# Kernel optimization log

Measured on AMD Instinct MI355X. Metric: run time of the kernel, lower is better.

Reference implementation:

```python
import jax, jax.numpy as jnp
import numpy as np

M = 16                      # multiplicity of each irrep block
INV3 = 1.0 / np.sqrt(3.0)   # w3j(1,1,0) component-normalized
INV2 = 1.0 / np.sqrt(2.0)   # w3j(1,1,1) component-normalized
A0 = 1.0 / np.sqrt(2.0 * M) # fan-in norm for 0e outputs (2 paths x mul 16)
A1 = 1.0 / np.sqrt(3.0 * M) # fan-in norm for 1o outputs (3 paths x mul 16)


def setup_inputs() -> dict:
    E, N, ED, HID = 100000, 10000, 32, 128
    WNUM = 2 * M * (2 * M) + 3 * M * M  # 1792 per-edge TP weights
    ks = jax.random.split(jax.random.key(0), 10)
    return {
        "dst": jax.random.randint(ks[0], (E,), 0, N),
        "x_src": jax.random.normal(ks[1], (E, 4 * M), jnp.float32),   # 16x0e+16x1o
        "x_dst": jax.random.normal(ks[2], (N, 4 * M), jnp.float32),
        "sh": jax.random.normal(ks[3], (E, 4), jnp.float32),          # 1x0e+1x1o
        "edge_attr": jax.random.normal(ks[4], (E, ED), jnp.float32),
        "We1": jax.random.normal(ks[5], (ED, HID), jnp.float32) / np.sqrt(ED),
        "be1": jnp.zeros((HID,), jnp.float32),
        "We2": jax.random.normal(ks[6], (HID, WNUM), jnp.float32) / np.sqrt(HID),
        "be2": jnp.zeros((WNUM,), jnp.float32),
        "Wr0": jax.random.normal(ks[7], (M, 2 * M), jnp.float32),     # 16x0e -> 32x0e
        "Wr1": jax.random.normal(ks[8], (M, M), jnp.float32),         # 16x1o -> 16x1o
    }


def _forward(dst, x_src, x_dst, sh, edge_attr, We1, be1, We2, be2, Wr0, Wr1):
    E = x_src.shape[0]
    N = x_dst.shape[0]
    o0 = 2 * M  # 32x0e tp output (scalars + gates)

    # edge MLP -> per-edge tensor-product weights [E, 1792]
    w = jax.nn.relu(edge_attr @ We1 + be1) @ We2 + be2
    i = 0
    w_ss = w[:, i:i + M * o0].reshape(E, M, o0); i += M * o0   # 0e x 0e -> 0e
    w_vv0 = w[:, i:i + M * o0].reshape(E, M, o0); i += M * o0  # 1o x 1o -> 0e
    w_sv = w[:, i:i + M * M].reshape(E, M, M); i += M * M      # 0e x 1o -> 1o
    w_vs = w[:, i:i + M * M].reshape(E, M, M); i += M * M      # 1o x 0e -> 1o
    w_vv1 = w[:, i:i + M * M].reshape(E, M, M)                 # 1o x 1o -> 1o

    s1 = x_src[:, :M]                       # [E, 16]
    v1 = x_src[:, M:].reshape(E, M, 3)      # [E, 16, 3]
    s2 = sh[:, 0]                           # [E]
    v2 = sh[:, 1:4]                         # [E, 3]

    # fully-connected tensor product with per-edge weights
    out0 = A0 * (jnp.einsum('em,emo->eo', s1 * s2[:, None], w_ss)
                 + INV3 * jnp.einsum('emc,ec,emo->eo', v1, v2, w_vv0))  # [E, 32]
    cross = jnp.cross(v1, v2[:, None, :])   # [E, 16, 3]
    out1 = A1 * (jnp.einsum('em,ec,emo->eoc', s1, v2, w_sv)
                 + jnp.einsum('emc,e,emo->eoc', v1, s2, w_vs)
                 + INV2 * jnp.einsum('emc,emo->eoc', cross, w_vv1))     # [E, 16, 3]
    msg = jnp.concatenate([out0, out1.reshape(E, -1)], axis=1)          # [E, 80]

    # scatter-mean over destination nodes
    ssum = jax.ops.segment_sum(msg, dst, num_segments=N)
    cnt = jax.ops.segment_sum(jnp.ones((E,), msg.dtype), dst, num_segments=N)
    msg = ssum / jnp.maximum(cnt, 1.0)[:, None]                          # [N, 80]

    # residual equivariant linear on x_dst
    sd = x_dst[:, :M]
    vd = x_dst[:, M:].reshape(N, M, 3)
    res0 = (sd @ Wr0) / np.sqrt(M)                                       # [N, 32]
    res1 = jnp.einsum('nmc,mo->noc', vd, Wr1) / np.sqrt(M)               # [N, 16, 3]
    msg = msg + jnp.concatenate([res0, res1.reshape(N, -1)], axis=1)

    # gate nonlinearity: relu(scalars), sigmoid(gates) * gated vectors
    scalars = jax.nn.relu(msg[:, :M])
    gates = jax.nn.sigmoid(msg[:, M:2 * M])
    gated = msg[:, 2 * M:].reshape(N, M, 3) * gates[:, :, None]
    return jnp.concatenate([scalars, gated.reshape(N, -1)], axis=1)      # [N, 64]


def reference(dst, x_src, x_dst, sh, edge_attr, We1, be1, We2, be2, Wr0, Wr1):
    return _forward(dst, x_src, x_dst, sh, edge_attr, We1, be1, We2, be2, Wr0, Wr1)
```

## Files before the change

### kernel.cpp

```cpp
#include <hip/hip_runtime.h>
#include <math.h>

#define WNUM 1792
#define HID 128

#define INV3C 0.5773502691896258f
#define INV2C 0.7071067811865476f
#define A0C   0.17677669529663687f
#define A1C   0.14433756729740643f
#define MAXDEG 64

typedef short bf8 __attribute__((ext_vector_type(8)));
typedef _Float16 f16x8 __attribute__((ext_vector_type(8)));
typedef _Float16 f16x4 __attribute__((ext_vector_type(4)));
typedef float f32x4 __attribute__((ext_vector_type(4)));

__device__ inline unsigned short f2bf(float f) {
  union { float f; unsigned u; } v; v.f = f;
  unsigned r = v.u + 0x7FFFu + ((v.u >> 16) & 1u);
  return (unsigned short)(r >> 16);
}
__device__ inline float bf2f(unsigned short h) {
  union { unsigned u; float f; } v; v.u = ((unsigned)h) << 16;
  return v.f;
}
__device__ inline float wscale(int t) {
  if (t < 32) return A0C;
  if (t < 64) return A0C * INV3C;
  if (t < 96) return A1C;
  return A1C * INV2C;
}

__global__ __launch_bounds__(256) void prep_kernel(
    const float* __restrict__ We1, const float* __restrict__ We2,
    const float* __restrict__ be2,
    unsigned short* __restrict__ we1x, _Float16* __restrict__ we2h,
    float* __restrict__ be2p, int* __restrict__ cntp, int N)
{
  int i = blockIdx.x * 256 + threadIdx.x;
  if (i < 28672) {
    int t = i >> 8, c = (i >> 6) & 3, lane = i & 63;
    int quad = lane >> 4, l15 = lane & 15;
    int col = t * 16 + l15;
    float sc = wscale(t);
    f16x8 v;
    #pragma unroll
    for (int j = 0; j < 8; ++j) {
      int k = c * 32 + quad * 8 + j;
      v[j] = (_Float16)(We2[(size_t)k * WNUM + col] * sc);
    }
    *(f16x8*)(we2h + (size_t)t * 2048 + c * 512 + lane * 8) = v;
  } else if (i < 29184) {
    int q = i - 28672;
    int c1 = q >> 6, lane = q & 63;
    int quad = lane >> 4, l15 = lane & 15;
    int col = c1 * 16 + l15;
    bf8 hh, ll;
    #pragma unroll
    for (int j = 0; j < 8; ++j) {
      int k = quad * 8 + j;
      float v = We1[k * HID + col];
      unsigned short hi = f2bf(v);
      hh[j] = (short)hi;
      ll[j] = (short)f2bf(v - bf2f(hi));
    }
    *(bf8*)(we1x + c1 * 1024 + lane * 8) = hh;
    *(bf8*)(we1x + c1 * 1024 + 512 + lane * 8) = ll;
  } else if (i < 30976) {
    int q = i - 29184;
    int t = q >> 4, l16 = q & 15;
    be2p[(t >> 1) * 32 + l16 * 2 + (t & 1)] = be2[q] * wscale(t);
  } else if (i < 30976 + N) {
    cntp[i - 30976] = 0;
  }
}

__device__ inline void chains2(const f16x8* a0, const f16x8* a1,
    const f16x8* b, float2 bias, f32x4* wa, f32x4* wb)
{
  f32x4 ca0 = {bias.x, bias.x, bias.x, bias.x};
  f32x4 cb0 = {bias.y, bias.y, bias.y, bias.y};
  f32x4 ca1 = ca0, cb1 = cb0;
  ca0 = __builtin_amdgcn_mfma_f32_16x16x32_f16(a0[0], b[0], ca0, 0, 0, 0);
  cb0 = __builtin_amdgcn_mfma_f32_16x16x32_f16(a0[0], b[4], cb0, 0, 0, 0);
  ca1 = __builtin_amdgcn_mfma_f32_16x16x32_f16(a1[0], b[0], ca1, 0, 0, 0);
  cb1 = __builtin_amdgcn_mfma_f32_16x16x32_f16(a1[0], b[4], cb1, 0, 0, 0);
  ca0 = __builtin_amdgcn_mfma_f32_16x16x32_f16(a0[1], b[1], ca0, 0, 0, 0);
  cb0 = __builtin_amdgcn_mfma_f32_16x16x32_f16(a0[1], b[5], cb0, 0, 0, 0);
  ca1 = __builtin_amdgcn_mfma_f32_16x16x32_f16(a1[1], b[1], ca1, 0, 0, 0);
  cb1 = __builtin_amdgcn_mfma_f32_16x16x32_f16(a1[1], b[5], cb1, 0, 0, 0);
  ca0 = __builtin_amdgcn_mfma_f32_16x16x32_f16(a0[2], b[2], ca0, 0, 0, 0);
  cb0 = __builtin_amdgcn_mfma_f32_16x16x32_f16(a0[2], b[6], cb0, 0, 0, 0);
  ca1 = __builtin_amdgcn_mfma_f32_16x16x32_f16(a1[2], b[2], ca1, 0, 0, 0);
  cb1 = __builtin_amdgcn_mfma_f32_16x16x32_f16(a1[2], b[6], cb1, 0, 0, 0);
  ca0 = __builtin_amdgcn_mfma_f32_16x16x32_f16(a0[3], b[3], ca0, 0, 0, 0);
  cb0 = __builtin_amdgcn_mfma_f32_16x16x32_f16(a0[3], b[7], cb0, 0, 0, 0);
  ca1 = __builtin_amdgcn_mfma_f32_16x16x32_f16(a1[3], b[3], ca1, 0, 0, 0);
  cb1 = __builtin_amdgcn_mfma_f32_16x16x32_f16(a1[3], b[7], cb1, 0, 0, 0);
  wa[0] = ca0; wb[0] = cb0; wa[1] = ca1; wb[1] = cb1;
}

__device__ inline void loadB8(const _Float16* __restrict__ bG, f16x8* b) {
  b[0] = *(const f16x8*)(bG);
  b[1] = *(const f16x8*)(bG + 512);
  b[2] = *(const f16x8*)(bG + 1024);
  b[3] = *(const f16x8*)(bG + 1536);
  b[4] = *(const f16x8*)(bG + 2048);
  b[5] = *(const f16x8*)(bG + 2560);
  b[6] = *(const f16x8*)(bG + 3072);
  b[7] = *(const f16x8*)(bG + 3584);
}

template <bool MSG>
__global__ __launch_bounds__(256, 2) void edge_kernel(
    const float* __restrict__ ea, const float* __restrict__ xsrc,
    const float* __restrict__ sh, const int* __restrict__ dst,
    const float* __restrict__ be1,
    const unsigned short* __restrict__ we1x, const _Float16* __restrict__ we2h,
    const float* __restrict__ be2p,
    float* __restrict__ outp, int* __restrict__ eidx, int* __restrict__ cntp, int E)
{
  const int lane = threadIdx.x & 63;
  const int w    = threadIdx.x >> 6;
  const int quad = lane >> 4;
  const int l16  = lane & 15;
  const int eb   = (blockIdx.x * 4 + w) * 32;

  __shared__ _Float16 h_s[4][16][136];
  __shared__ _Float16 s1h_s[4][16][32];
  __shared__ _Float16 v1h_s[4][16][3][32];
  __shared__ float4 vq_s[4][32];

  if (lane < 32) {
    int ge = eb + lane;
    if (ge < E) {
      int node = dst[ge];
      int pos = atomicAdd(cntp + node, 1);
      if (MSG) { if (pos < MAXDEG) eidx[node * MAXDEG + pos] = ge; }
    }
  }

  {
    int e2 = lane >> 1, mg = lane & 1;
    int ge = eb + e2;
    if (ge < E) {
      const float* xp = xsrc + (size_t)ge * 64;
      float4 sq0 = *(const float4*)(xp + mg * 8);
      float4 sq1 = *(const float4*)(xp + mg * 8 + 4);
      float s1a[8] = {sq0.x,sq0.y,sq0.z,sq0.w,sq1.x,sq1.y,sq1.z,sq1.w};
      const float* vp = xp + 16 + mg * 24;
      float la[24];
      #pragma unroll
      for (int qv = 0; qv < 6; ++qv) {
        float4 t = *(const float4*)(vp + qv * 4);
        la[qv*4+0] = t.x; la[qv*4+1] = t.y; la[qv*4+2] = t.z; la[qv*4+3] = t.w;
      }
      float4 shq = *(const float4*)(sh + (size_t)ge * 4);
      float s2 = shq.x, v2x = shq.y, v2y = shq.z, v2z = shq.w;
      #pragma unroll
      for (int mi = 0; mi < 8; ++mi) {
        int m = mg * 8 + mi;
        float v1x = la[mi*3], v1y = la[mi*3+1], v1z = la[mi*3+2];
        s1h_s[w][m][e2] = (_Float16)s1a[mi];
        v1h_s[w][m][0][e2] = (_Float16)v1x;
        v1h_s[w][m][1][e2] = (_Float16)v1y;
        v1h_s[w][m][2][e2] = (_Float16)v1z;
      }
      if (mg == 0) vq_s[w][e2] = make_float4(v2x, v2y, v2z, s2);
    } else {
      #pragma unroll
      for (int mi = 0; mi < 8; ++mi) {
        int m = mg * 8 + mi;
        s1h_s[w][m][e2] = (_Float16)0.f;
        v1h_s[w][m][0][e2] = (_Float16)0.f;
        v1h_s[w][m][1][e2] = (_Float16)0.f;
        v1h_s[w][m][2][e2] = (_Float16)0.f;
      }
      if (mg == 0) vq_s[w][e2] = make_float4(0,0,0,0);
    }
  }

  f16x8 af[2][4];
  {
    const unsigned short* wb1 = we1x + lane * 8;
    #pragma unroll
    for (int g = 0; g < 2; ++g) {
      bf8 ah, al;
      {
        int gea = eb + g * 16 + l16; if (gea > E - 1) gea = E - 1;
        const float* ep = ea + (size_t)gea * 32 + quad * 8;
        float4 p0 = *(const float4*)ep;
        float4 p1 = *(const float4*)(ep + 4);
        float pv[8] = {p0.x,p0.y,p0.z,p0.w,p1.x,p1.y,p1.z,p1.w};
        #pragma unroll
        for (int j = 0; j < 8; ++j) {
          unsigned short hi = f2bf(pv[j]);
          ah[j] = (short)hi;
          al[j] = (short)f2bf(pv[j] - bf2f(hi));
        }
      }
      #pragma unroll 2
      for (int c = 0; c < 8; ++c) {
        bf8 bh = *(const bf8*)(wb1 + c * 1024);
        bf8 bl = *(const bf8*)(wb1 + c * 1024 + 512);
        float bias = be1[c * 16 + l16];
        f32x4 hc = {bias, bias, bias, bias};
        hc = __builtin_amdgcn_mfma_f32_16x16x32_bf16(al, bh, hc, 0, 0, 0);
        hc = __builtin_amdgcn_mfma_f32_16x16x32_bf16(ah, bl, hc, 0, 0, 0);
        hc = __builtin_amdgcn_mfma_f32_16x16x32_bf16(ah, bh, hc, 0, 0, 0);
        #pragma unroll
        for (int r = 0; r < 4; ++r)
          h_s[w][quad * 4 + r][c * 16 + l16] = (_Float16)fmaxf(hc[r], 0.f);
      }
      #pragma unroll
      for (int ch = 0; ch < 4; ++ch)
        af[g][ch] = *(const f16x8*)&h_s[w][l16][ch * 32 + quad * 8];
      asm volatile("s_waitcnt lgkmcnt(0)" ::: "memory");
      __builtin_amdgcn_sched_barrier(0);
    }
  }

  const float* bp = be2p + l16 * 2;
  const _Float16* bG0 = we2h + lane * 8;
  float m0a[2][4] = {{0,0,0,0},{0,0,0,0}}, m0b[2][4] = {{0,0,0,0},{0,0,0,0}};

  f16x8 bufA[8], bufB[8];
  loadB8(bG0, bufA);

  {
    float s2v[2][4];
    #pragma unroll
    for (int g = 0; g < 2; ++g)
      #pragma unroll
      for (int r = 0; r < 4; ++r)
        s2v[g][r] = vq_s[w][g * 16 + quad * 4 + r].w;

    #pragma unroll 1
    for (int i = 0; i < 16; i += 2) {
      loadB8(bG0 + (size_t)(i + 1) * 4096, bufB);
      f32x4 wa[2], wb[2];
      chains2(af[0], af[1], bufA, *(const float2*)(bp + i * 32), wa, wb);
      #pragma unroll
      for (int g = 0; g < 2; ++g) {
        f16x4 fv = *(const f16x4*)&s1h_s[w][i][g * 16 + quad * 4];
        #pragma unroll
        for (int r = 0; r < 4; ++r) {
          float f = (float)fv[r] * s2v[g][r];
          m0a[g][r] = fmaf(wa[g][r], f, m0a[g][r]);
          m0b[g][r] = fmaf(wb[g][r], f, m0b[g][r]);
        }
      }
      loadB8(bG0 + (size_t)(i + 2) * 4096, bufA);
      chains2(af[0], af[1], bufB, *(const float2*)(bp + (i + 1) * 32), wa, wb);
      #pragma unroll
      for (int g = 0; g < 2; ++g) {
        f16x4 fv = *(const f16x4*)&s1h_s[w][i + 1][g * 16 + quad * 4];
        #pragma unroll
        for (int r = 0; r < 4; ++r) {
          float f = (float)fv[r] * s2v[g][r];
          m0a[g][r] = fmaf(wa[g][r], f, m0a[g][r]);
          m0b[g][r] = fmaf(wb[g][r], f, m0b[g][r]);
        }
      }
    }
  }

  {
    float v2xv[2][4], v2yv[2][4], v2zv[2][4];
    #pragma unroll
    for (int g = 0; g < 2; ++g)
      #pragma unroll
      for (int r = 0; r < 4; ++r) {
        float4 q = vq_s[w][g * 16 + quad * 4 + r];
        v2xv[g][r] = q.x; v2yv[g][r] = q.y; v2zv[g][r] = q.z;
      }

    #pragma unroll 1
    for (int i = 0; i < 16; i += 2) {
      int pg = 16 + i;
      loadB8(bG0 + (size_t)(pg + 1) * 4096, bufB);
      f32x4 wa[2], wb[2];
      chains2(af[0], af[1], bufA, *(const float2*)(bp + pg * 32), wa, wb);
      #pragma unroll
      for (int g = 0; g < 2; ++g) {
        f16x4 xA = *(const f16x4*)&v1h_s[w][i][0][g * 16 + quad * 4];
        f16x4 yA = *(const f16x4*)&v1h_s[w][i][1][g * 16 + quad * 4];
        f16x4 zA = *(const f16x4*)&v1h_s[w][i][2][g * 16 + quad * 4];
        #pragma unroll
        for (int r = 0; r < 4; ++r) {
          float f = fmaf((float)zA[r], v2zv[g][r],
                    fmaf((float)yA[r], v2yv[g][r], (float)xA[r] * v2xv[g][r]));
          m0a[g][r] = fmaf(wa[g][r], f, m0a[g][r]);
          m0b[g][r] = fmaf(wb[g][r], f, m0b[g][r]);
        }
      }
      loadB8(bG0 + (size_t)(pg + 2) * 4096, bufA);
      chains2(af[0], af[1], bufB, *(const float2*)(bp + (pg + 1) * 32), wa, wb);
      #pragma unroll
      for (int g = 0; g < 2; ++g) {
        f16x4 xA = *(const f16x4*)&v1h_s[w][i + 1][0][g * 16 + quad * 4];
        f16x4 yA = *(const f16x4*)&v1h_s[w][i + 1][1][g * 16 + quad * 4];
        f16x4 zA = *(const f16x4*)&v1h_s[w][i + 1][2][g * 16 + quad * 4];
        #pragma unroll
        for (int r = 0; r < 4; ++r) {
          float f = fmaf((float)zA[r], v2zv[g][r],
                    fmaf((float)yA[r], v2yv[g][r], (float)xA[r] * v2xv[g][r]));
          m0a[g][r] = fmaf(wa[g][r], f, m0a[g][r]);
          m0b[g][r] = fmaf(wb[g][r], f, m0b[g][r]);
        }
      }
    }
  }

  #pragma unroll
  for (int g = 0; g < 2; ++g)
    #pragma unroll
    for (int r = 0; r < 4; ++r) {
      int ge = eb + g * 16 + quad * 4 + r;
      if (ge < E) {
        if (MSG) {
          float* mp = outp + (size_t)ge * 80;
          mp[l16]      = m0a[g][r];
          mp[16 + l16] = m0b[g][r];
        } else {
          float* ap = outp + (size_t)dst[ge] * 80;
          atomicAdd(ap + l16,      m0a[g][r]);
          atomicAdd(ap + 16 + l16, m0b[g][r]);
        }
      }
    }

  float sg[2][4] = {{0,0,0,0},{0,0,0,0}};
  #pragma unroll 1
  for (int i = 0; i < 8; i += 2) {
    int pg = 32 + i;
    loadB8(bG0 + (size_t)(pg + 1) * 4096, bufB);
    f32x4 wa[2], wb[2];
    chains2(af[0], af[1], bufA, *(const float2*)(bp + pg * 32), wa, wb);
    #pragma unroll
    for (int g = 0; g < 2; ++g) {
      f16x4 sA = *(const f16x4*)&s1h_s[w][2*i][g * 16 + quad * 4];
      f16x4 sB = *(const f16x4*)&s1h_s[w][2*i + 1][g * 16 + quad * 4];
      #pragma unroll
      for (int r = 0; r < 4; ++r)
        sg[g][r] = fmaf(wb[g][r], (float)sB[r], fmaf(wa[g][r], (float)sA[r], sg[g][r]));
    }
    loadB8(bG0 + (size_t)(pg + 2) * 4096, bufA);
    chains2(af[0], af[1], bufB, *(const float2*)(bp + (pg + 1) * 32), wa, wb);
    #pragma unroll
    for (int g = 0; g < 2; ++g) {
      f16x4 sA = *(const f16x4*)&s1h_s[w][2*i + 2][g * 16 + quad * 4];
      f16x4 sB = *(const f16x4*)&s1h_s[w][2*i + 3][g * 16 + quad * 4];
      #pragma unroll
      for (int r = 0; r < 4; ++r)
        sg[g][r] = fmaf(wb[g][r], (float)sB[r], fmaf(wa[g][r], (float)sA[r], sg[g][r]));
    }
  }
  float4 vq[2][4];
  #pragma unroll
  for (int g = 0; g < 2; ++g)
    #pragma unroll
    for (int r = 0; r < 4; ++r) vq[g][r] = vq_s[w][g * 16 + quad * 4 + r];

  float m1x[2][4], m1y[2][4], m1z[2][4];
  #pragma unroll
  for (int g = 0; g < 2; ++g)
    #pragma unroll
    for (int r = 0; r < 4; ++r) {
      m1x[g][r] = sg[g][r] * vq[g][r].x;
      m1y[g][r] = sg[g][r] * vq[g][r].y;
      m1z[g][r] = sg[g][r] * vq[g][r].z;
    }

  #pragma unroll
  for (int sec = 0; sec < 2; ++sec) {
    float ux[2][4] = {{0,0,0,0},{0,0,0,0}}, uy[2][4] = {{0,0,0,0},{0,0,0,0}},
          uz[2][4] = {{0,0,0,0},{0,0,0,0}};
    int base = 40 + sec * 8;
    #pragma unroll 1
    for (int i = 0; i < 8; i += 2) {
      int pg = base + i;
      loadB8(bG0 + (size_t)(pg + 1) * 4096, bufB);
      f32x4 wa[2], wb[2];
      chains2(af[0], af[1], bufA, *(const float2*)(bp + pg * 32), wa, wb);
      #pragma unroll
      for (int g = 0; g < 2; ++g) {
        f16x4 xA = *(const f16x4*)&v1h_s[w][2*i][0][g*16 + quad*4];
        f16x4 xB = *(const f16x4*)&v1h_s[w][2*i+1][0][g*16 + quad*4];
        f16x4 yA = *(const f16x4*)&v1h_s[w][2*i][1][g*16 + quad*4];
        f16x4 yB = *(const f16x4*)&v1h_s[w][2*i+1][1][g*16 + quad*4];
        f16x4 zA = *(const f16x4*)&v1h_s[w][2*i][2][g*16 + quad*4];
        f16x4 zB = *(const f16x4*)&v1h_s[w][2*i+1][2][g*16 + quad*4];
        #pragma unroll
        for (int r = 0; r < 4; ++r) {
          ux[g][r] = fmaf(wb[g][r], (float)xB[r], fmaf(wa[g][r], (float)xA[r], ux[g][r]));
          uy[g][r] = fmaf(wb[g][r], (float)yB[r], fmaf(wa[g][r], (float)yA[r], uy[g][r]));
          uz[g][r] = fmaf(wb[g][r], (float)zB[r], fmaf(wa[g][r], (float)zA[r], uz[g][r]));
        }
      }
      {
        int pn = pg + 2; if (pn > 55) pn = 55;
        loadB8(bG0 + (size_t)pn * 4096, bufA);
      }
      chains2(af[0], af[1], bufB, *(const float2*)(bp + (pg + 1) * 32), wa, wb);
      #pragma unroll
      for (int g = 0; g < 2; ++g) {
        f16x4 xA = *(const f16x4*)&v1h_s[w][2*i+2][0][g*16 + quad*4];
        f16x4 xB = *(const f16x4*)&v1h_s[w][2*i+3][0][g*16 + quad*4];
        f16x4 yA = *(const f16x4*)&v1h_s[w][2*i+2][1][g*16 + quad*4];
        f16x4 yB = *(const f16x4*)&v1h_s[w][2*i+3][1][g*16 + quad*4];
        f16x4 zA = *(const f16x4*)&v1h_s[w][2*i+2][2][g*16 + quad*4];
        f16x4 zB = *(const f16x4*)&v1h_s[w][2*i+3][2][g*16 + quad*4];
        #pragma unroll
        for (int r = 0; r < 4; ++r) {
          ux[g][r] = fmaf(wb[g][r], (float)xB[r], fmaf(wa[g][r], (float)xA[r], ux[g][r]));
          uy[g][r] = fmaf(wb[g][r], (float)yB[r], fmaf(wa[g][r], (float)yA[r], uy[g][r]));
          uz[g][r] = fmaf(wb[g][r], (float)zB[r], fmaf(wa[g][r], (float)zA[r], uz[g][r]));
        }
      }
    }
    if (sec == 0) {
      #pragma unroll
      for (int g = 0; g < 2; ++g)
        #pragma unroll
        for (int r = 0; r < 4; ++r) {
          m1x[g][r] = fmaf(vq[g][r].w, ux[g][r], m1x[g][r]);
          m1y[g][r] = fmaf(vq[g][r].w, uy[g][r], m1y[g][r]);
          m1z[g][r] = fmaf(vq[g][r].w, uz[g][r], m1z[g][r]);
        }
    } else {
      #pragma unroll
      for (int g = 0; g < 2; ++g)
        #pragma unroll
        for (int r = 0; r < 4; ++r) {
          m1x[g][r] = fmaf(uy[g][r], vq[g][r].z, m1x[g][r]);
          m1x[g][r] = fmaf(-uz[g][r], vq[g][r].y, m1x[g][r]);
          m1y[g][r] = fmaf(uz[g][r], vq[g][r].x, m1y[g][r]);
          m1y[g][r] = fmaf(-ux[g][r], vq[g][r].z, m1y[g][r]);
          m1z[g][r] = fmaf(ux[g][r], vq[g][r].y, m1z[g][r]);
          m1z[g][r] = fmaf(-uy[g][r], vq[g][r].x, m1z[g][r]);
        }
    }
  }

  #pragma unroll
  for (int g = 0; g < 2; ++g)
    #pragma unroll
    for (int r = 0; r < 4; ++r) {
      int ge = eb + g * 16 + quad * 4 + r;
      if (ge < E) {
        if (MSG) {
          float* mp = outp + (size_t)ge * 80;
          mp[32 + l16*3 + 0] = m1x[g][r];
          mp[32 + l16*3 + 1] = m1y[g][r];
          mp[32 + l16*3 + 2] = m1z[g][r];
        } else {
          float* ap = outp + (size_t)dst[ge] * 80;
          atomicAdd(ap + 32 + l16*3 + 0, m1x[g][r]);
          atomicAdd(ap + 32 + l16*3 + 1, m1y[g][r]);
          atomicAdd(ap + 32 + l16*3 + 2, m1z[g][r]);
        }
      }
    }
}

__global__ __launch_bounds__(128) void node_gather_kernel(
    const float* __restrict__ msg, const int* __restrict__ eidx,
    const int* __restrict__ cntp,
    const float* __restrict__ xdst, const float* __restrict__ Wr0,
    const float* __restrict__ Wr1, float* __restrict__ out, int N)
{
  int n = blockIdx.x;
  if (n >= N) return;
  int j = threadIdx.x;
  int c0 = cntp[n];
  int deg = c0 < MAXDEG ? c0 : MAXDEG;
  float inv = 1.0f / fmaxf((float)c0, 1.0f);
  __shared__ float s_sum[80];
  if (j < 80) {
    float s = 0.f;
    const int* ep = eidx + (size_t)n * MAXDEG;
    int i = 0;
    for (; i + 1 < deg; i += 2) {
      int e0 = ep[i], e1 = ep[i + 1];
      s += msg[(size_t)e0 * 80 + j] + msg[(size_t)e1 * 80 + j];
    }
    if (i < deg) s += msg[(size_t)ep[i] * 80 + j];
    s_sum[j] = s * inv;
  }
  __syncthreads();
  if (j >= 64) return;
  const float* xd = xdst + (size_t)n * 64;
  float* op = out + (size_t)n * 64;
  if (j < 16) {
    float s = 0.f;
    #pragma unroll
    for (int m = 0; m < 16; ++m) s = fmaf(xd[m], Wr0[m * 32 + j], s);
    op[j] = fmaxf(s_sum[j] + 0.25f * s, 0.f);
  } else {
    int jj = j - 16;
    int o = (jj * 86) >> 8;
    int c = jj - o * 3;
    float tg = 0.f, v = 0.f;
    #pragma unroll
    for (int m = 0; m < 16; ++m) {
      tg = fmaf(xd[m], Wr0[m * 32 + 16 + o], tg);
      v  = fmaf(xd[16 + m * 3 + c], Wr1[m * 16 + o], v);
    }
    float g = 1.0f / (1.0f + expf(-(s_sum[16 + o] + 0.25f * tg)));
    op[16 + jj] = (s_sum[32 + jj] + 0.25f * v) * g;
  }
}

__global__ __launch_bounds__(256) void node_kernel(
    const float* __restrict__ accn, const int* __restrict__ cntp,
    const float* __restrict__ xdst, const float* __restrict__ Wr0,
    const float* __restrict__ Wr1, float* __restrict__ out, int N)
{
  int idx = blockIdx.x * 256 + threadIdx.x;
  int n = idx >> 6, j = idx & 63;
  if (n >= N) return;
  float inv = 1.0f / fmaxf((float)cntp[n], 1.0f);
  const float* ap = accn + (size_t)n * 80;
  const float* xd = xdst + (size_t)n * 64;
  float* op = out + (size_t)n * 64;
  if (j < 16) {
    float s = 0.f;
    #pragma unroll
    for (int m = 0; m < 16; ++m) s = fmaf(xd[m], Wr0[m * 32 + j], s);
    op[j] = fmaxf(ap[j] * inv + 0.25f * s, 0.f);
  } else {
    int jj = j - 16;
    int o = (jj * 86) >> 8;
    int c = jj - o * 3;
    float tg = 0.f, v = 0.f;
    #pragma unroll
    for (int m = 0; m < 16; ++m) {
      tg = fmaf(xd[m], Wr0[m * 32 + 16 + o], tg);
      v  = fmaf(xd[16 + m * 3 + c], Wr1[m * 16 + o], v);
    }
    float g = 1.0f / (1.0f + expf(-(ap[16 + o] * inv + 0.25f * tg)));
    op[16 + jj] = (ap[32 + jj] * inv + 0.25f * v) * g;
  }
}

extern "C" void kernel_launch(void* const* d_in, const int* in_sizes, int n_in,
                              void* d_out, int out_size, void* d_ws, size_t ws_size,
                              hipStream_t stream)
{
  const int*   dst  = (const int*)d_in[0];
  const float* xsrc = (const float*)d_in[1];
  const float* xdst = (const float*)d_in[2];
  const float* sh   = (const float*)d_in[3];
  const float* ea   = (const float*)d_in[4];
  const float* We1  = (const float*)d_in[5];
  const float* be1  = (const float*)d_in[6];
  const float* We2  = (const float*)d_in[7];
  const float* be2  = (const float*)d_in[8];
  const float* Wr0  = (const float*)d_in[9];
  const float* Wr1  = (const float*)d_in[10];
  const int E = in_sizes[0];
  const int N = in_sizes[2] / 64;

  char* ws = (char*)d_ws;
  _Float16* we2h = (_Float16*)ws;
  unsigned short* we1x = (unsigned short*)(ws + 458752);
  float* be2p = (float*)(ws + 475136);
  int*   cntp = (int*)(ws + 482560);
  size_t off = 482560 + (size_t)N * 4;
  off = (off + 15) & ~(size_t)15;

  size_t need_msg = off + (size_t)N * MAXDEG * 4 + (size_t)E * 80 * 4;
  bool use_msg = (ws_size >= need_msg);

  prep_kernel<<<(30976 + N + 255) / 256, 256, 0, stream>>>(We1, We2, be2,
      we1x, we2h, be2p, cntp, N);

  if (use_msg) {
    int* eidx = (int*)(ws + off);
    float* msg = (float*)(ws + off + (size_t)N * MAXDEG * 4);
    edge_kernel<true><<<(E + 127) / 128, 256, 0, stream>>>(ea, xsrc, sh, dst, be1,
        we1x, we2h, be2p, msg, eidx, cntp, E);
    node_gather_kernel<<<N, 128, 0, stream>>>(msg, eidx, cntp, xdst, Wr0, Wr1,
        (float*)d_out, N);
  } else {
    float* accn = (float*)(ws + off);
    hipMemsetAsync(accn, 0, (size_t)N * 320, stream);
    edge_kernel<false><<<(E + 127) / 128, 256, 0, stream>>>(ea, xsrc, sh, dst, be1,
        we1x, we2h, be2p, accn, (int*)nullptr, cntp, E);
    node_kernel<<<((size_t)N * 64 + 255) / 256, 256, 0, stream>>>(accn, cntp,
        xdst, Wr0, Wr1, (float*)d_out, N);
  }
}
```

Before: 206.5 us.

## Process 64 edges per wave to reuse each We2 fragment across four MFMA groups

Each wave now handles 64 edges instead of 32, so every loaded We2 B-fragment feeds four 16-edge MFMA groups rather than two, which halves the B traffic per edge. The manual double buffering of B fragments is dropped in favour of a simple per-iteration load. The launch bound falls to one block per SM, and the sh vector data is read straight from global memory instead of through a shared staging array. The cross-product combination is deferred to the epilogue using separate accumulators. The cost is much higher register pressure and lower occupancy, and memory latency is no longer hidden by explicit prefetching.

```diff
diff --git a/kernel.cpp b/kernel.cpp
--- a/kernel.cpp
+++ b/kernel.cpp
@@ -112,7 +112,7 @@
 }
 
 template <bool MSG>
-__global__ __launch_bounds__(256, 2) void edge_kernel(
+__global__ __launch_bounds__(256, 1) void edge_kernel(
     const float* __restrict__ ea, const float* __restrict__ xsrc,
     const float* __restrict__ sh, const int* __restrict__ dst,
     const float* __restrict__ be1,
@@ -124,14 +124,13 @@
   const int w    = threadIdx.x >> 6;
   const int quad = lane >> 4;
   const int l16  = lane & 15;
-  const int eb   = (blockIdx.x * 4 + w) * 32;
+  const int eb   = (blockIdx.x * 4 + w) * 64;
 
   __shared__ _Float16 h_s[4][16][136];
-  __shared__ _Float16 s1h_s[4][16][32];
-  __shared__ _Float16 v1h_s[4][16][3][32];
-  __shared__ float4 vq_s[4][32];
-
-  if (lane < 32) {
+  __shared__ _Float16 s1h_s[4][16][64];
+  __shared__ _Float16 v1h_s[4][16][3][64];
+
+  {
     int ge = eb + lane;
     if (ge < E) {
       int node = dst[ge];
@@ -141,50 +140,44 @@
   }
 
   {
-    int e2 = lane >> 1, mg = lane & 1;
-    int ge = eb + e2;
+    int ge = eb + lane;
     if (ge < E) {
       const float* xp = xsrc + (size_t)ge * 64;
-      float4 sq0 = *(const float4*)(xp + mg * 8);
-      float4 sq1 = *(const float4*)(xp + mg * 8 + 4);
-      float s1a[8] = {sq0.x,sq0.y,sq0.z,sq0.w,sq1.x,sq1.y,sq1.z,sq1.w};
-      const float* vp = xp + 16 + mg * 24;
-      float la[24];
-      #pragma unroll
-      for (int qv = 0; qv < 6; ++qv) {
-        float4 t = *(const float4*)(vp + qv * 4);
-        la[qv*4+0] = t.x; la[qv*4+1] = t.y; la[qv*4+2] = t.z; la[qv*4+3] = t.w;
-      }
-      float4 shq = *(const float4*)(sh + (size_t)ge * 4);
-      float s2 = shq.x, v2x = shq.y, v2y = shq.z, v2z = shq.w;
-      #pragma unroll
-      for (int mi = 0; mi < 8; ++mi) {
-        int m = mg * 8 + mi;
-        float v1x = la[mi*3], v1y = la[mi*3+1], v1z = la[mi*3+2];
-        s1h_s[w][m][e2] = (_Float16)s1a[mi];
-        v1h_s[w][m][0][e2] = (_Float16)v1x;
-        v1h_s[w][m][1][e2] = (_Float16)v1y;
-        v1h_s[w][m][2][e2] = (_Float16)v1z;
-      }
-      if (mg == 0) vq_s[w][e2] = make_float4(v2x, v2y, v2z, s2);
+      float s1a[16];
+      #pragma unroll
+      for (int q = 0; q < 4; ++q) {
+        float4 t = *(const float4*)(xp + q * 4);
+        s1a[q*4+0] = t.x; s1a[q*4+1] = t.y; s1a[q*4+2] = t.z; s1a[q*4+3] = t.w;
+      }
+      float la[48];
+      #pragma unroll
+      for (int q = 0; q < 12; ++q) {
+        float4 t = *(const float4*)(xp + 16 + q * 4);
+        la[q*4+0] = t.x; la[q*4+1] = t.y; la[q*4+2] = t.z; la[q*4+3] = t.w;
+      }
+      #pragma unroll
+      for (int m = 0; m < 16; ++m) {
+        s1h_s[w][m][lane] = (_Float16)s1a[m];
+        v1h_s[w][m][0][lane] = (_Float16)la[m*3];
+        v1h_s[w][m][1][lane] = (_Float16)la[m*3+1];
+        v1h_s[w][m][2][lane] = (_Float16)la[m*3+2];
+      }
     } else {
       #pragma unroll
-      for (int mi = 0; mi < 8; ++mi) {
-        int m = mg * 8 + mi;
-        s1h_s[w][m][e2] = (_Float16)0.f;
-        v1h_s[w][m][0][e2] = (_Float16)0.f;
-        v1h_s[w][m][1][e2] = (_Float16)0.f;
-        v1h_s[w][m][2][e2] = (_Float16)0.f;
-      }
-      if (mg == 0) vq_s[w][e2] = make_float4(0,0,0,0);
-    }
-  }
-
-  f16x8 af[2][4];
+      for (int m = 0; m < 16; ++m) {
+        s1h_s[w][m][lane] = (_Float16)0.f;
+        v1h_s[w][m][0][lane] = (_Float16)0.f;
+        v1h_s[w][m][1][lane] = (_Float16)0.f;
+        v1h_s[w][m][2][lane] = (_Float16)0.f;
+      }
+    }
+  }
+
+  f16x8 af[4][4];
   {
     const unsigned short* wb1 = we1x + lane * 8;
     #pragma unroll
-    for (int g = 0; g < 2; ++g) {
+    for (int g = 0; g < 4; ++g) {
       bf8 ah, al;
       {
         int gea = eb + g * 16 + l16; if (gea > E - 1) gea = E - 1;
@@ -222,98 +215,84 @@
 
   const float* bp = be2p + l16 * 2;
   const _Float16* bG0 = we2h + lane * 8;
-  float m0a[2][4] = {{0,0,0,0},{0,0,0,0}}, m0b[2][4] = {{0,0,0,0},{0,0,0,0}};
-
-  f16x8 bufA[8], bufB[8];
-  loadB8(bG0, bufA);
+  float m0a[4][4], m0b[4][4];
+  #pragma unroll
+  for (int g = 0; g < 4; ++g)
+    #pragma unroll
+    for (int r = 0; r < 4; ++r) { m0a[g][r] = 0.f; m0b[g][r] = 0.f; }
 
   {
-    float s2v[2][4];
-    #pragma unroll
-    for (int g = 0; g < 2; ++g)
-      #pragma unroll
-      for (int r = 0; r < 4; ++r)
-        s2v[g][r] = vq_s[w][g * 16 + quad * 4 + r].w;
+    float s2v[4][4];
+    #pragma unroll
+    for (int g = 0; g < 4; ++g)
+      #pragma unroll
+      for (int r = 0; r < 4; ++r) {
+        int gev = eb + g * 16 + quad * 4 + r; if (gev > E - 1) gev = E - 1;
+        s2v[g][r] = sh[(size_t)gev * 4];
+      }
 
     #pragma unroll 1
-    for (int i = 0; i < 16; i += 2) {
-      loadB8(bG0 + (size_t)(i + 1) * 4096, bufB);
-      f32x4 wa[2], wb[2];
-      chains2(af[0], af[1], bufA, *(const float2*)(bp + i * 32), wa, wb);
-      #pragma unroll
-      for (int g = 0; g < 2; ++g) {
-        f16x4 fv = *(const f16x4*)&s1h_s[w][i][g * 16 + quad * 4];
-        #pragma unroll
-        for (int r = 0; r < 4; ++r) {
-          float f = (float)fv[r] * s2v[g][r];
-          m0a[g][r] = fmaf(wa[g][r], f, m0a[g][r]);
-          m0b[g][r] = fmaf(wb[g][r], f, m0b[g][r]);
-        }
-      }
-      loadB8(bG0 + (size_t)(i + 2) * 4096, bufA);
-      chains2(af[0], af[1], bufB, *(const float2*)(bp + (i + 1) * 32), wa, wb);
-      #pragma unroll
-      for (int g = 0; g < 2; ++g) {
-        f16x4 fv = *(const f16x4*)&s1h_s[w][i + 1][g * 16 + quad * 4];
-        #pragma unroll
-        for (int r = 0; r < 4; ++r) {
-          float f = (float)fv[r] * s2v[g][r];
-          m0a[g][r] = fmaf(wa[g][r], f, m0a[g][r]);
-          m0b[g][r] = fmaf(wb[g][r], f, m0b[g][r]);
+    for (int i = 0; i < 16; ++i) {
+      f16x8 b[8]; loadB8(bG0 + (size_t)i * 4096, b);
+      float2 bias2 = *(const float2*)(bp + i * 32);
+      #pragma unroll
+      for (int hh = 0; hh < 2; ++hh) {
+        f32x4 wa[2], wb[2];
+        chains2(af[2*hh], af[2*hh+1], b, bias2, wa, wb);
+        #pragma unroll
+        for (int gg = 0; gg < 2; ++gg) {
+          f16x4 fv = *(const f16x4*)&s1h_s[w][i][(2*hh+gg) * 16 + quad * 4];
+          #pragma unroll
+          for (int r = 0; r < 4; ++r) {
+            float f = (float)fv[r] * s2v[2*hh+gg][r];
+            m0a[2*hh+gg][r] = fmaf(wa[gg][r], f, m0a[2*hh+gg][r]);
+            m0b[2*hh+gg][r] = fmaf(wb[gg][r], f, m0b[2*hh+gg][r]);
+          }
         }
       }
     }
   }
 
   {
-    float v2xv[2][4], v2yv[2][4], v2zv[2][4];
-    #pragma unroll
-    for (int g = 0; g < 2; ++g)
+    float v2xv[4][4], v2yv[4][4], v2zv[4][4];
+    #pragma unroll
+    for (int g = 0; g < 4; ++g)
       #pragma unroll
       for (int r = 0; r < 4; ++r) {
-        float4 q = vq_s[w][g * 16 + quad * 4 + r];
-        v2xv[g][r] = q.x; v2yv[g][r] = q.y; v2zv[g][r] = q.z;
+        int gev = eb + g * 16 + quad * 4 + r; if (gev > E - 1) gev = E - 1;
+        const float* sp = sh + (size_t)gev * 4;
+        v2xv[g][r] = sp[1]; v2yv[g][r] = sp[2]; v2zv[g][r] = sp[3];
       }
 
     #pragma unroll 1
-    for (int i = 0; i < 16; i += 2) {
+    for (int i = 0; i < 16; ++i) {
       int pg = 16 + i;
-      loadB8(bG0 + (size_t)(pg + 1) * 4096, bufB);
-      f32x4 wa[2], wb[2];
-      chains2(af[0], af[1], bufA, *(const float2*)(bp + pg * 32), wa, wb);
-      #pragma unroll
-      for (int g = 0; g < 2; ++g) {
-        f16x4 xA = *(const f16x4*)&v1h_s[w][i][0][g * 16 + quad * 4];
-        f16x4 yA = *(const f16x4*)&v1h_s[w][i][1][g * 16 + quad * 4];
-        f16x4 zA = *(const f16x4*)&v1h_s[w][i][2][g * 16 + quad * 4];
-        #pragma unroll
-        for (int r = 0; r < 4; ++r) {
-          float f = fmaf((float)zA[r], v2zv[g][r],
-                    fmaf((float)yA[r], v2yv[g][r], (float)xA[r] * v2xv[g][r]));
-          m0a[g][r] = fmaf(wa[g][r], f, m0a[g][r]);
-          m0b[g][r] = fmaf(wb[g][r], f, m0b[g][r]);
-        }
-      }
-      loadB8(bG0 + (size_t)(pg + 2) * 4096, bufA);
-      chains2(af[0], af[1], bufB, *(const float2*)(bp + (pg + 1) * 32), wa, wb);
-      #pragma unroll
-      for (int g = 0; g < 2; ++g) {
-        f16x4 xA = *(const f16x4*)&v1h_s[w][i + 1][0][g * 16 + quad * 4];
-        f16x4 yA = *(const f16x4*)&v1h_s[w][i + 1][1][g * 16 + quad * 4];
-        f16x4 zA = *(const f16x4*)&v1h_s[w][i + 1][2][g * 16 + quad * 4];
-        #pragma unroll
-        for (int r = 0; r < 4; ++r) {
-          float f = fmaf((float)zA[r], v2zv[g][r],
-                    fmaf((float)yA[r], v2yv[g][r], (float)xA[r] * v2xv[g][r]));
-          m0a[g][r] = fmaf(wa[g][r], f, m0a[g][r]);
-          m0b[g][r] = fmaf(wb[g][r], f, m0b[g][r]);
+      f16x8 b[8]; loadB8(bG0 + (size_t)pg * 4096, b);
+      float2 bias2 = *(const float2*)(bp + pg * 32);
+      #pragma unroll
+      for (int hh = 0; hh < 2; ++hh) {
+        f32x4 wa[2], wb[2];
+        chains2(af[2*hh], af[2*hh+1], b, bias2, wa, wb);
+        #pragma unroll
+        for (int gg = 0; gg < 2; ++gg) {
+          int g = 2*hh + gg;
+          f16x4 xA = *(const f16x4*)&v1h_s[w][i][0][g * 16 + quad * 4];
+          f16x4 yA = *(const f16x4*)&v1h_s[w][i][1][g * 16 + quad * 4];
+          f16x4 zA = *(const f16x4*)&v1h_s[w][i][2][g * 16 + quad * 4];
+          #pragma unroll
+          for (int r = 0; r < 4; ++r) {
+            float f = fmaf((float)zA[r], v2zv[g][r],
+                      fmaf((float)yA[r], v2yv[g][r], (float)xA[r] * v2xv[g][r]));
+            m0a[g][r] = fmaf(wa[gg][r], f, m0a[g][r]);
+            m0b[g][r] = fmaf(wb[gg][r], f, m0b[g][r]);
+          }
         }
       }
     }
   }
 
   #pragma unroll
-  for (int g = 0; g < 2; ++g)
+  for (int g = 0; g < 4; ++g)
     #pragma unroll
     for (int r = 0; r < 4; ++r) {
       int ge = eb + g * 16 + quad * 4 + r;
@@ -330,61 +309,50 @@
       }
     }
 
-  float sg[2][4] = {{0,0,0,0},{0,0,0,0}};
+  float sg[4][4];
+  #pragma unroll
+  for (int g = 0; g < 4; ++g)
+    #pragma unroll
+    for (int r = 0; r < 4; ++r) sg[g][r] = 0.f;
   #pragma unroll 1
-  for (int i = 0; i < 8; i += 2) {
+  for (int i = 0; i < 8; ++i) {
     int pg = 32 + i;
-    loadB8(bG0 + (size_t)(pg + 1) * 4096, bufB);
-    f32x4 wa[2], wb[2];
-    chains2(af[0], af[1], bufA, *(const float2*)(bp + pg * 32), wa, wb);
-    #pragma unroll
-    for (int g = 0; g < 2; ++g) {
-      f16x4 sA = *(const f16x4*)&s1h_s[w][2*i][g * 16 + quad * 4];
-      f16x4 sB = *(const f16x4*)&s1h_s[w][2*i + 1][g * 16 + quad * 4];
-      #pragma unroll
-      for (int r = 0; r < 4; ++r)
-        sg[g][r] = fmaf(wb[g][r], (float)sB[r], fmaf(wa[g][r], (float)sA[r], sg[g][r]));
-    }
-    loadB8(bG0 + (size_t)(pg + 2) * 4096, bufA);
-    chains2(af[0], af[1], bufB, *(const float2*)(bp + (pg + 1) * 32), wa, wb);
-    #pragma unroll
-    for (int g = 0; g < 2; ++g) {
-      f16x4 sA = *(const f16x4*)&s1h_s[w][2*i + 2][g * 16 + quad * 4];
-      f16x4 sB = *(const f16x4*)&s1h_s[w][2*i + 3][g * 16 + quad * 4];
-      #pragma unroll
-      for (int r = 0; r < 4; ++r)
-        sg[g][r] = fmaf(wb[g][r], (float)sB[r], fmaf(wa[g][r], (float)sA[r], sg[g][r]));
-    }
-  }
-  float4 vq[2][4];
+    f16x8 b[8]; loadB8(bG0 + (size_t)pg * 4096, b);
+    float2 bias2 = *(const float2*)(bp + pg * 32);
+    #pragma unroll
+    for (int hh = 0; hh < 2; ++hh) {
+      f32x4 wa[2], wb[2];
+      chains2(af[2*hh], af[2*hh+1], b, bias2, wa, wb);
+      #pragma unroll
+      for (int gg = 0; gg < 2; ++gg) {
+        int g = 2*hh + gg;
+        f16x4 sA = *(const f16x4*)&s1h_s[w][2*i][g * 16 + quad * 4];
+        f16x4 sB = *(const f16x4*)&s1h_s[w][2*i + 1][g * 16 + quad * 4];
+        #pragma unroll
+        for (int r = 0; r < 4; ++r)
+          sg[g][r] = fmaf(wb[gg][r], (float)sB[r],
+                     fmaf(wa[gg][r], (float)sA[r], sg[g][r]));
+      }
+    }
+  }
+
+  float uSx[4][4], uSy[4][4], uSz[4][4];
   #pragma unroll
-  for (int g = 0; g < 2; ++g)
-    #pragma unroll
-    for (int r = 0; r < 4; ++r) vq[g][r] = vq_s[w][g * 16 + quad * 4 + r];
-
-  float m1x[2][4], m1y[2][4], m1z[2][4];
-  #pragma unroll
-  for (int g = 0; g < 2; ++g)
-    #pragma unroll
-    for (int r = 0; r < 4; ++r) {
-      m1x[g][r] = sg[g][r] * vq[g][r].x;
-      m1y[g][r] = sg[g][r] * vq[g][r].y;
-      m1z[g][r] = sg[g][r] * vq[g][r].z;
-    }
-
-  #pragma unroll
-  for (int sec = 0; sec < 2; ++sec) {
-    float ux[2][4] = {{0,0,0,0},{0,0,0,0}}, uy[2][4] = {{0,0,0,0},{0,0,0,0}},
-          uz[2][4] = {{0,0,0,0},{0,0,0,0}};
-    int base = 40 + sec * 8;
-    #pragma unroll 1
-    for (int i = 0; i < 8; i += 2) {
-      int pg = base + i;
-      loadB8(bG0 + (size_t)(pg + 1) * 4096, bufB);
+  for (int g = 0; g < 4; ++g)
+    #pragma unroll
+    for (int r = 0; r < 4; ++r) { uSx[g][r]=0.f; uSy[g][r]=0.f; uSz[g][r]=0.f; }
+  #pragma unroll 1
+  for (int i = 0; i < 8; ++i) {
+    int pg = 40 + i;
+    f16x8 b[8]; loadB8(bG0 + (size_t)pg * 4096, b);
+    float2 bias2 = *(const float2*)(bp + pg * 32);
+    #pragma unroll
+    for (int hh = 0; hh < 2; ++hh) {
       f32x4 wa[2], wb[2];
-      chains2(af[0], af[1], bufA, *(const float2*)(bp + pg * 32), wa, wb);
-      #pragma unroll
-      for (int g = 0; g < 2; ++g) {
+      chains2(af[2*hh], af[2*hh+1], b, bias2, wa, wb);
+      #pragma unroll
+      for (int gg = 0; gg < 2; ++gg) {
+        int g = 2*hh + gg;
         f16x4 xA = *(const f16x4*)&v1h_s[w][2*i][0][g*16 + quad*4];
         f16x4 xB = *(const f16x4*)&v1h_s[w][2*i+1][0][g*16 + quad*4];
         f16x4 yA = *(const f16x4*)&v1h_s[w][2*i][1][g*16 + quad*4];
@@ -393,72 +361,71 @@
         f16x4 zB = *(const f16x4*)&v1h_s[w][2*i+1][2][g*16 + quad*4];
         #pragma unroll
         for (int r = 0; r < 4; ++r) {
-          ux[g][r] = fmaf(wb[g][r], (float)xB[r], fmaf(wa[g][r], (float)xA[r], ux[g][r]));
-          uy[g][r] = fmaf(wb[g][r], (float)yB[r], fmaf(wa[g][r], (float)yA[r], uy[g][r]));
-          uz[g][r] = fmaf(wb[g][r], (float)zB[r], fmaf(wa[g][r], (float)zA[r], uz[g][r]));
-        }
-      }
-      {
-        int pn = pg + 2; if (pn > 55) pn = 55;
-        loadB8(bG0 + (size_t)pn * 4096, bufA);
-      }
-      chains2(af[0], af[1], bufB, *(const float2*)(bp + (pg + 1) * 32), wa, wb);
-      #pragma unroll
-      for (int g = 0; g < 2; ++g) {
-        f16x4 xA = *(const f16x4*)&v1h_s[w][2*i+2][0][g*16 + quad*4];
-        f16x4 xB = *(const f16x4*)&v1h_s[w][2*i+3][0][g*16 + quad*4];
-        f16x4 yA = *(const f16x4*)&v1h_s[w][2*i+2][1][g*16 + quad*4];
-        f16x4 yB = *(const f16x4*)&v1h_s[w][2*i+3][1][g*16 + quad*4];
-        f16x4 zA = *(const f16x4*)&v1h_s[w][2*i+2][2][g*16 + quad*4];
-        f16x4 zB = *(const f16x4*)&v1h_s[w][2*i+3][2][g*16 + quad*4];
+          uSx[g][r] = fmaf(wb[gg][r], (float)xB[r], fmaf(wa[gg][r], (float)xA[r], uSx[g][r]));
+          uSy[g][r] = fmaf(wb[gg][r], (float)yB[r], fmaf(wa[gg][r], (float)yA[r], uSy[g][r]));
+          uSz[g][r] = fmaf(wb[gg][r], (float)zB[r], fmaf(wa[gg][r], (float)zA[r], uSz[g][r]));
+        }
+      }
+    }
+  }
+
+  float uCx[4][4], uCy[4][4], uCz[4][4];
+  #pragma unroll
+  for (int g = 0; g < 4; ++g)
+    #pragma unroll
+    for (int r = 0; r < 4; ++r) { uCx[g][r]=0.f; uCy[g][r]=0.f; uCz[g][r]=0.f; }
+  #pragma unroll 1
+  for (int i = 0; i < 8; ++i) {
+    int pg = 48 + i;
+    f16x8 b[8]; loadB8(bG0 + (size_t)pg * 4096, b);
+    float2 bias2 = *(const float2*)(bp + pg * 32);
+    #pragma unroll
+    for (int hh = 0; hh < 2; ++hh) {
+      f32x4 wa[2], wb[2];
+      chains2(af[2*hh], af[2*hh+1], b, bias2, wa, wb);
+      #pragma unroll
+      for (int gg = 0; gg < 2; ++gg) {
+        int g = 2*hh + gg;
+        f16x4 xA = *(const f16x4*)&v1h_s[w][2*i][0][g*16 + quad*4];
+        f16x4 xB = *(const f16x4*)&v1h_s[w][2*i+1][0][g*16 + quad*4];
+        f16x4 yA = *(const f16x4*)&v1h_s[w][2*i][1][g*16 + quad*4];
+        f16x4 yB = *(const f16x4*)&v1h_s[w][2*i+1][1][g*16 + quad*4];
+        f16x4 zA = *(const f16x4*)&v1h_s[w][2*i][2][g*16 + quad*4];
+        f16x4 zB = *(const f16x4*)&v1h_s[w][2*i+1][2][g*16 + quad*4];
         #pragma unroll
         for (int r = 0; r < 4; ++r) {
-          ux[g][r] = fmaf(wb[g][r], (float)xB[r], fmaf(wa[g][r], (float)xA[r], ux[g][r]));
-          uy[g][r] = fmaf(wb[g][r], (float)yB[r], fmaf(wa[g][r], (float)yA[r], uy[g][r]));
-          uz[g][r] = fmaf(wb[g][r], (float)zB[r], fmaf(wa[g][r], (float)zA[r], uz[g][r]));
-        }
-      }
-    }
-    if (sec == 0) {
-      #pragma unroll
-      for (int g = 0; g < 2; ++g)
-        #pragma unroll
-        for (int r = 0; r < 4; ++r) {
-          m1x[g][r] = fmaf(vq[g][r].w, ux[g][r], m1x[g][r]);
-          m1y[g][r] = fmaf(vq[g][r].w, uy[g][r], m1y[g][r]);
-          m1z[g][r] = fmaf(vq[g][r].w, uz[g][r], m1z[g][r]);
-        }
-    } else {
-      #pragma unroll
-      for (int g = 0; g < 2; ++g)
-        #pragma unroll
-        for (int r = 0; r < 4; ++r) {
-          m1x[g][r] = fmaf(uy[g][r], vq[g][r].z, m1x[g][r]);
-          m1x[g][r] = fmaf(-uz[g][r], vq[g][r].y, m1x[g][r]);
-          m1y[g][r] = fmaf(uz[g][r], vq[g][r].x, m1y[g][r]);
-          m1y[g][r] = fmaf(-ux[g][r], vq[g][r].z, m1y[g][r]);
-          m1z[g][r] = fmaf(ux[g][r], vq[g][r].y, m1z[g][r]);
-          m1z[g][r] = fmaf(-uy[g][r], vq[g][r].x, m1z[g][r]);
-        }
+          uCx[g][r] = fmaf(wb[gg][r], (float)xB[r], fmaf(wa[gg][r], (float)xA[r], uCx[g][r]));
+          uCy[g][r] = fmaf(wb[gg][r], (float)yB[r], fmaf(wa[gg][r], (float)yA[r], uCy[g][r]));
+          uCz[g][r] = fmaf(wb[gg][r], (float)zB[r], fmaf(wa[gg][r], (float)zA[r], uCz[g][r]));
+        }
+      }
     }
   }
 
   #pragma unroll
-  for (int g = 0; g < 2; ++g)
+  for (int g = 0; g < 4; ++g)
     #pragma unroll
     for (int r = 0; r < 4; ++r) {
       int ge = eb + g * 16 + quad * 4 + r;
       if (ge < E) {
+        float4 q = *(const float4*)(sh + (size_t)ge * 4);
+        float s2 = q.x, v2x = q.y, v2y = q.z, v2z = q.w;
+        float mx = fmaf(sg[g][r], v2x, fmaf(s2, uSx[g][r],
+                   fmaf(uCy[g][r], v2z, -uCz[g][r] * v2y)));
+        float my = fmaf(sg[g][r], v2y, fmaf(s2, uSy[g][r],
+                   fmaf(uCz[g][r], v2x, -uCx[g][r] * v2z)));
+        float mz = fmaf(sg[g][r], v2z, fmaf(s2, uSz[g][r],
+                   fmaf(uCx[g][r], v2y, -uCy[g][r] * v2x)));
         if (MSG) {
           float* mp = outp + (size_t)ge * 80;
-          mp[32 + l16*3 + 0] = m1x[g][r];
-          mp[32 + l16*3 + 1] = m1y[g][r];
-          mp[32 + l16*3 + 2] = m1z[g][r];
+          mp[32 + l16*3 + 0] = mx;
+          mp[32 + l16*3 + 1] = my;
+          mp[32 + l16*3 + 2] = mz;
         } else {
           float* ap = outp + (size_t)dst[ge] * 80;
-          atomicAdd(ap + 32 + l16*3 + 0, m1x[g][r]);
-          atomicAdd(ap + 32 + l16*3 + 1, m1y[g][r]);
-          atomicAdd(ap + 32 + l16*3 + 2, m1z[g][r]);
+          atomicAdd(ap + 32 + l16*3 + 0, mx);
+          atomicAdd(ap + 32 + l16*3 + 1, my);
+          atomicAdd(ap + 32 + l16*3 + 2, mz);
         }
       }
     }
@@ -579,14 +546,14 @@
   if (use_msg) {
     int* eidx = (int*)(ws + off);
     float* msg = (float*)(ws + off + (size_t)N * MAXDEG * 4);
-    edge_kernel<true><<<(E + 127) / 128, 256, 0, stream>>>(ea, xsrc, sh, dst, be1,
+    edge_kernel<true><<<(E + 255) / 256, 256, 0, stream>>>(ea, xsrc, sh, dst, be1,
         we1x, we2h, be2p, msg, eidx, cntp, E);
     node_gather_kernel<<<N, 128, 0, stream>>>(msg, eidx, cntp, xdst, Wr0, Wr1,
         (float*)d_out, N);
   } else {
     float* accn = (float*)(ws + off);
     hipMemsetAsync(accn, 0, (size_t)N * 320, stream);
-    edge_kernel<false><<<(E + 127) / 128, 256, 0, stream>>>(ea, xsrc, sh, dst, be1,
+    edge_kernel<false><<<(E + 255) / 256, 256, 0, stream>>>(ea, xsrc, sh, dst, be1,
         we1x, we2h, be2p, accn, (int*)nullptr, cntp, E);
     node_kernel<<<((size_t)N * 64 + 255) / 256, 256, 0, stream>>>(accn, cntp,
         xdst, Wr0, Wr1, (float*)d_out, N);
```

Result: slower. 248.3 us (+20.2%).
